# Performance work log

Measured on AMD Instinct MI355X. Metric: run time of the kernel, lower is better.

The kernel has to match this reference:

```python
import jax, jax.numpy as jnp
import numpy as np

SEED_SPACING = 0.06      # eps for DBSCAN
MIN_SAMPLES = 3          # sklearn counts the point itself
MAX_SUPERPOINTS = 512


def _dbscan_superpoints(coords):
    """DBSCAN(eps, min_samples=3) on [N,3] coords + the module's relabeling.

    Connected components over the eps-graph restricted to core points are
    found by min-index label propagation (with pointer jumping) inside a
    while_loop; border points take the min core-neighbor label; noise is
    filled with the most common label; labels are compacted and capped at
    MAX_SUPERPOINTS exactly as in the torch module. Returns [N] int32.
    """
    N = coords.shape[0]
    SENT = N  # sentinel label meaning "no cluster / noise"

    # pairwise squared euclidean distances via GEMM
    sq = jnp.sum(coords * coords, axis=-1)                      # [N]
    d2 = sq[:, None] + sq[None, :] - 2.0 * (coords @ coords.T)  # [N,N]
    adj = d2 <= SEED_SPACING * SEED_SPACING                     # includes self
    core = jnp.sum(adj, axis=-1) >= MIN_SAMPLES                 # [N] bool

    idx = jnp.arange(N)
    core_col = core[None, :]

    def step(l):
        # min label among core neighbors
        nb = jnp.min(jnp.where(adj & core_col, l[None, :], SENT), axis=-1)
        l2 = jnp.where(core, jnp.minimum(l, nb), SENT)
        # pointer jumping: labels are indices of core points, so l2[l2] is valid
        safe = jnp.where(l2 < N, l2, 0)
        l2 = jnp.where(l2 < N, jnp.minimum(l2, l2[safe]), SENT)
        return l2

    def cond(state):
        return state[1]

    def body(state):
        l, _ = state
        l_new = step(l)
        return l_new, jnp.any(l_new != l)

    l0 = jnp.where(core, idx, SENT)
    l_final, _ = jax.lax.while_loop(cond, body, (l0, jnp.array(True)))

    # border points: min label of any core neighbor; else stay noise
    border = jnp.min(jnp.where(adj & core_col, l_final[None, :], SENT), axis=-1)
    labels = jnp.where(core, l_final, border)

    # noise fill: assign most common valid label (or 0 if none valid)
    noise = labels == SENT
    safe_lab = jnp.where(noise, 0, labels)
    counts = jnp.zeros(N, jnp.int32).at[safe_lab].add(jnp.where(noise, 0, 1))
    any_valid = jnp.any(~noise)
    most_common = jnp.argmax(counts).astype(labels.dtype)
    labels = jnp.where(noise, jnp.where(any_valid, most_common, 0), labels)

    # compact to consecutive ids ordered by min point index (== first occurrence)
    present = jnp.zeros(N, bool).at[labels].set(True)
    rank = (jnp.cumsum(present) - 1).astype(labels.dtype)
    labels = rank[labels]
    n_clusters = jnp.sum(present)

    # cap at MAX_SUPERPOINTS: keep the MAX largest clusters, rest -> 0
    counts2 = jnp.zeros(N, jnp.int32).at[labels].add(1)
    top = jnp.argsort(counts2)[-MAX_SUPERPOINTS:]
    remap = jnp.zeros(N, labels.dtype).at[top].set(
        jnp.arange(MAX_SUPERPOINTS, dtype=labels.dtype))
    labels = jnp.where(n_clusters > MAX_SUPERPOINTS, remap[labels], labels)
    return labels.astype(jnp.int32)


def setup_inputs() -> dict:
    key = jax.random.key(0)
    coordinates = jax.random.uniform(key, (8, 4096, 3), dtype=jnp.float32)
    return {"coordinates": coordinates}


def reference(coordinates):
    # [B, N, 3] -> [B, N] int32 superpoint labels
    return jax.vmap(_dbscan_superpoints)(coordinates)
```

## Files before the change

kernel.cpp:

```cpp
#include <hip/hip_runtime.h>
#include <stdint.h>

#define NPTS 4096
#define SENT NPTS
#define MAXSP 512
#define ECAP 65536
#define ECACHE 16384

typedef unsigned long long ull;

__device__ __forceinline__ int find_lds(int* p, int x){
  while (true){
    int px = p[x];
    if (px == x) return x;
    int ppx = p[px];
    if (ppx == px) return px;
    p[x] = ppx;
    x = ppx;
  }
}

__device__ __forceinline__ void union_lds(int* p, int a, int b){
  a = find_lds(p, a);
  b = find_lds(p, b);
  while (a != b){
    int lo = min(a, b), hi = max(a, b);
    int old = atomicCAS(&p[hi], hi, lo);
    if (old == hi || old == lo) return;
    a = lo; b = old;
  }
}

__device__ __forceinline__ ull trimask(ull m, int i, int base){
  if (base + 63 <= i) return 0ULL;
  if (base <= i) return m & ((~0ULL) << (i - base + 1));
  return m;
}

__global__ void k_prep(const float* __restrict__ coords,
                       float4* __restrict__ pts,
                       int* __restrict__ ecnt, int batches){
#pragma clang fp contract(off)
  int g = blockIdx.x * blockDim.x + threadIdx.x;
  if (blockIdx.x == 0 && threadIdx.x < batches) ecnt[threadIdx.x << 6] = 0;
  float x = coords[g*3+0], y = coords[g*3+1], z = coords[g*3+2];
  float sq = ((x*x) + (y*y)) + (z*z);
  pts[g] = make_float4(x, y, z, sq);
}

__global__ void k_adj(const float4* __restrict__ pts,
                      uint32_t* __restrict__ edges,
                      int* __restrict__ ecnt){
#pragma clang fp contract(off)
  __shared__ int sTot, sBase;
  int tid  = threadIdx.x;
  int wv   = (blockIdx.x * blockDim.x + tid) >> 6;
  int lane = tid & 63;
  int b = wv >> 9;
  int m = wv & 511;
  int i0 = m << 2;
  int h0 = (NPTS - 4) - i0;
  const float4* pb = pts + (b << 12);
  if (tid == 0) sTot = 0;
  __syncthreads();
  const float EPS2 = (float)(0.06 * 0.06);
  float4 pL[4], pH[4];
  #pragma unroll
  for (int r = 0; r < 4; ++r){ pL[r] = pb[i0 + r]; pH[r] = pb[h0 + r]; }
  ull wl[4] = {0,0,0,0}, wh[4] = {0,0,0,0};
  int base = lane << 6;
  {
    int W = i0 >> 6;
    float4 pj = pb[(W << 6) + lane];
    for (int k = W; k < 64; ++k){
      float4 cur = pj;
      if (k + 1 < 64) pj = pb[((k + 1) << 6) + lane];
      #pragma unroll
      for (int r = 0; r < 4; ++r){
        float dot = __builtin_fmaf(pL[r].z, cur.z,
                    __builtin_fmaf(pL[r].y, cur.y, pL[r].x * cur.x));
        float d2  = __builtin_fmaf(-2.0f, dot, pL[r].w + cur.w);
        ull bal = __ballot(d2 <= EPS2);
        if (lane == k) wl[r] = bal;
      }
    }
  }
  {
    int W = h0 >> 6;
    float4 pj = pb[(W << 6) + lane];
    for (int k = W; k < 64; ++k){
      float4 cur = pj;
      if (k + 1 < 64) pj = pb[((k + 1) << 6) + lane];
      #pragma unroll
      for (int r = 0; r < 4; ++r){
        float dot = __builtin_fmaf(pH[r].z, cur.z,
                    __builtin_fmaf(pH[r].y, cur.y, pH[r].x * cur.x));
        float d2  = __builtin_fmaf(-2.0f, dot, pH[r].w + cur.w);
        ull bal = __ballot(d2 <= EPS2);
        if (lane == k) wh[r] = bal;
      }
    }
  }
  #pragma unroll
  for (int r = 0; r < 4; ++r){
    wl[r] = trimask(wl[r], i0 + r, base);
    wh[r] = trimask(wh[r], h0 + r, base);
  }
  int cnt = 0;
  #pragma unroll
  for (int r = 0; r < 4; ++r) cnt += __popcll(wl[r]) + __popcll(wh[r]);
  int incl = cnt;
  #pragma unroll
  for (int off = 1; off < 64; off <<= 1){
    int y = __shfl_up(incl, off);
    if (lane >= off) incl += y;
  }
  int total = __shfl(incl, 63);
  int woff = 0;
  if (lane == 63) woff = atomicAdd(&sTot, total);
  woff = __shfl(woff, 63);
  __syncthreads();
  if (tid == 0) sBase = atomicAdd(&ecnt[b << 6], sTot);
  __syncthreads();
  int pos = sBase + woff + incl - cnt;
  uint32_t* eb = edges + (size_t)b * ECAP;
  #define EMIT(mm, row) { ull e = (mm); while (e){ int bit = __builtin_ctzll(e); \
      e &= e - 1; if (pos < ECAP) eb[pos] = ((uint32_t)(row) << 12) | (uint32_t)(base + bit); ++pos; } }
  #pragma unroll
  for (int r = 0; r < 4; ++r) EMIT(wl[r], i0 + r)
  #pragma unroll
  for (int r = 0; r < 4; ++r) EMIT(wh[r], h0 + r)
  #undef EMIT
}

__global__ __launch_bounds__(1024) void k_mega(const uint32_t* __restrict__ edges,
                                               const int* __restrict__ ecnt,
                                               int* __restrict__ out){
  __shared__ int par[NPTS];
  __shared__ int LAB[NPTS];
  __shared__ unsigned char corea[NPTS];
  __shared__ uint32_t ec[ECACHE];
  __shared__ int wtots[16];
  __shared__ int sMost;
  int b = blockIdx.x, t = threadIdx.x;
  int wid = t >> 6, lane = t & 63;
  int cnt = min(ecnt[b << 6], ECAP);
  const uint32_t* eb = edges + (size_t)b * ECAP;
  for (int s = 0; s < 4; ++s){ int v = (t << 2) + s; par[v] = 0; }
  if (t == 0) sMost = -1;
  __syncthreads();
  for (int e = t; e < cnt; e += 1024){
    uint32_t pk = eb[e];
    if (e < ECACHE) ec[e] = pk;
    atomicAdd(&par[pk >> 12], 1);
    atomicAdd(&par[pk & 4095], 1);
  }
  __syncthreads();
  for (int s = 0; s < 4; ++s){ int v = (t << 2) + s; corea[v] = (par[v] >= 2) ? 1 : 0; }
  __syncthreads();
  for (int s = 0; s < 4; ++s){ int v = (t << 2) + s; par[v] = v; }
  __syncthreads();
  for (int e = t; e < cnt; e += 1024){
    uint32_t pk = (e < ECACHE) ? ec[e] : eb[e];
    int u = pk >> 12, v = pk & 4095;
    if (corea[u] && corea[v]) union_lds(par, u, v);
  }
  __syncthreads();
  for (int s = 0; s < 4; ++s){
    int v = (t << 2) + s;
    LAB[v] = corea[v] ? find_lds(par, v) : SENT;
  }
  __syncthreads();
  for (int e = t; e < cnt; e += 1024){
    uint32_t pk = (e < ECACHE) ? ec[e] : eb[e];
    int u = pk >> 12, v = pk & 4095;
    int cu = corea[u], cv = corea[v];
    if (cu && !cv)      atomicMin(&LAB[v], find_lds(par, u));
    else if (cv && !cu) atomicMin(&LAB[u], find_lds(par, v));
  }
  __syncthreads();
  int* A  = (int*)ec;
  int* Bb = A + NPTS;
  for (int s = 0; s < 4; ++s){ int v = (t << 2) + s; A[v] = 0; }
  __syncthreads();
  for (int s = 0; s < 4; ++s){ int l = LAB[(t << 2) + s]; if (l < SENT) atomicAdd(&A[l], 1); }
  __syncthreads();
  for (int s = 0; s < 4; ++s){
    int v = (t << 2) + s; int c = A[v];
    if (c > 0) atomicMax(&sMost, (c << 13) | (4095 - v));
  }
  __syncthreads();
  int most = (sMost >= 0) ? (4095 - (sMost & 8191)) : 0;
  for (int s = 0; s < 4; ++s){ int v = (t << 2) + s; if (LAB[v] == SENT) LAB[v] = most; Bb[v] = 0; }
  __syncthreads();
  for (int s = 0; s < 4; ++s) Bb[LAB[(t << 2) + s]] = 1;
  __syncthreads();
  int pv[4]; int ls = 0;
  for (int s = 0; s < 4; ++s){ pv[s] = Bb[(t << 2) + s]; ls += pv[s]; }
  int incl = ls;
  #pragma unroll
  for (int off = 1; off < 64; off <<= 1){
    int y = __shfl_up(incl, off);
    if (lane >= off) incl += y;
  }
  if (lane == 63) wtots[wid] = incl;
  __syncthreads();
  int wbase = 0, ncl = 0;
  #pragma unroll
  for (int w = 0; w < 16; ++w){
    int wt = wtots[w];
    if (w < wid) wbase += wt;
    ncl += wt;
  }
  int run = wbase + incl - ls;
  for (int s = 0; s < 4; ++s){ run += pv[s]; Bb[(t << 2) + s] = run - 1; }
  __syncthreads();
  for (int s = 0; s < 4; ++s){ int v = (t << 2) + s; LAB[v] = Bb[LAB[v]]; }
  __syncthreads();
  if (ncl > MAXSP){
    for (int s = 0; s < 4; ++s) A[(t << 2) + s] = 0;
    __syncthreads();
    for (int s = 0; s < 4; ++s) atomicAdd(&A[LAB[(t << 2) + s]], 1);
    __syncthreads();
    for (int v = t; v < ncl; v += 1024){
      int keyv = A[v] * NPTS + v;
      int p = 0;
      for (int u = 0; u < ncl; ++u) p += ((A[u] * NPTS + u) < keyv) ? 1 : 0;
      int full = p + (NPTS - ncl);
      Bb[v] = (full >= NPTS - MAXSP) ? (full - (NPTS - MAXSP)) : 0;
    }
    __syncthreads();
    for (int s = 0; s < 4; ++s){ int v = (t << 2) + s; LAB[v] = Bb[LAB[v]]; }
    __syncthreads();
  }
  int* og = out + (b << 12);
  for (int s = 0; s < 4; ++s){ int v = (t << 2) + s; og[v] = LAB[v]; }
}

extern "C" void kernel_launch(void* const* d_in, const int* in_sizes, int n_in,
                              void* d_out, int out_size, void* d_ws, size_t ws_size,
                              hipStream_t stream){
  const float* coords = (const float*)d_in[0];
  int* out = (int*)d_out;
  int batches = in_sizes[0] / (NPTS * 3);

  char* ws = (char*)d_ws;
  size_t off = 0;
  float4* pts = (float4*)(ws + off); off += (size_t)batches * NPTS * sizeof(float4);
  int* ecnt   = (int*)(ws + off);    off += (size_t)batches * 64 * sizeof(int);
  uint32_t* edges = (uint32_t*)(ws + off); off += (size_t)batches * ECAP * sizeof(uint32_t);

  int npts_all = batches * NPTS;
  k_prep<<<npts_all / 256, 256, 0, stream>>>(coords, pts, ecnt, batches);
  k_adj<<<npts_all / 32, 256, 0, stream>>>(pts, edges, ecnt);
  k_mega<<<batches, 1024, 0, stream>>>(edges, ecnt, out);
}
```

Before: 62.45 us.

## Fuse point prep into adjacency kernel and compute degrees with global atomics

Removes the separate prep kernel: the adjacency kernel now reads raw xyz coordinates and computes the squared norm on the fly. Per-point degree counting moves from an LDS atomic pass in the mega kernel to global atomics issued while edges are emitted, and a memset zeroes the degree and count buffers. The mega kernel drops its LDS edge cache and its first edge pass, reusing the parent array for histograms. The trade is heavier global atomic traffic, unaligned strided coordinate loads, and rereading edges from global memory in later passes.

After: 66.05 us. 1.06x slower.

```diff
diff --git a/kernel.cpp b/kernel.cpp
--- a/kernel.cpp
+++ b/kernel.cpp
@@ -5,7 +5,6 @@
 #define SENT NPTS
 #define MAXSP 512
 #define ECAP 65536
-#define ECACHE 16384
 
 typedef unsigned long long ull;
 
@@ -37,20 +36,17 @@
   return m;
 }
 
-__global__ void k_prep(const float* __restrict__ coords,
-                       float4* __restrict__ pts,
-                       int* __restrict__ ecnt, int batches){
+__device__ __forceinline__ float4 loadpt(const float* __restrict__ c, int g){
 #pragma clang fp contract(off)
-  int g = blockIdx.x * blockDim.x + threadIdx.x;
-  if (blockIdx.x == 0 && threadIdx.x < batches) ecnt[threadIdx.x << 6] = 0;
-  float x = coords[g*3+0], y = coords[g*3+1], z = coords[g*3+2];
+  float x = c[g*3+0], y = c[g*3+1], z = c[g*3+2];
   float sq = ((x*x) + (y*y)) + (z*z);
-  pts[g] = make_float4(x, y, z, sq);
-}
-
-__global__ void k_adj(const float4* __restrict__ pts,
+  return make_float4(x, y, z, sq);
+}
+
+__global__ void k_adj(const float* __restrict__ coords,
                       uint32_t* __restrict__ edges,
-                      int* __restrict__ ecnt){
+                      int* __restrict__ ecnt,
+                      int* __restrict__ deg){
 #pragma clang fp contract(off)
   __shared__ int sTot, sBase;
   int tid  = threadIdx.x;
@@ -60,21 +56,21 @@
   int m = wv & 511;
   int i0 = m << 2;
   int h0 = (NPTS - 4) - i0;
-  const float4* pb = pts + (b << 12);
+  const float* cb = coords + ((size_t)b << 12) * 3;
   if (tid == 0) sTot = 0;
   __syncthreads();
   const float EPS2 = (float)(0.06 * 0.06);
   float4 pL[4], pH[4];
   #pragma unroll
-  for (int r = 0; r < 4; ++r){ pL[r] = pb[i0 + r]; pH[r] = pb[h0 + r]; }
+  for (int r = 0; r < 4; ++r){ pL[r] = loadpt(cb, i0 + r); pH[r] = loadpt(cb, h0 + r); }
   ull wl[4] = {0,0,0,0}, wh[4] = {0,0,0,0};
   int base = lane << 6;
   {
     int W = i0 >> 6;
-    float4 pj = pb[(W << 6) + lane];
+    float4 pj = loadpt(cb, (W << 6) + lane);
     for (int k = W; k < 64; ++k){
       float4 cur = pj;
-      if (k + 1 < 64) pj = pb[((k + 1) << 6) + lane];
+      if (k + 1 < 64) pj = loadpt(cb, ((k + 1) << 6) + lane);
       #pragma unroll
       for (int r = 0; r < 4; ++r){
         float dot = __builtin_fmaf(pL[r].z, cur.z,
@@ -87,10 +83,10 @@
   }
   {
     int W = h0 >> 6;
-    float4 pj = pb[(W << 6) + lane];
+    float4 pj = loadpt(cb, (W << 6) + lane);
     for (int k = W; k < 64; ++k){
       float4 cur = pj;
-      if (k + 1 < 64) pj = pb[((k + 1) << 6) + lane];
+      if (k + 1 < 64) pj = loadpt(cb, ((k + 1) << 6) + lane);
       #pragma unroll
       for (int r = 0; r < 4; ++r){
         float dot = __builtin_fmaf(pH[r].z, cur.z,
@@ -124,8 +120,11 @@
   __syncthreads();
   int pos = sBase + woff + incl - cnt;
   uint32_t* eb = edges + (size_t)b * ECAP;
+  int* dg = deg + (b << 12);
   #define EMIT(mm, row) { ull e = (mm); while (e){ int bit = __builtin_ctzll(e); \
-      e &= e - 1; if (pos < ECAP) eb[pos] = ((uint32_t)(row) << 12) | (uint32_t)(base + bit); ++pos; } }
+      e &= e - 1; int j = base + bit; \
+      if (pos < ECAP) eb[pos] = ((uint32_t)(row) << 12) | (uint32_t)j; ++pos; \
+      atomicAdd(&dg[row], 1); atomicAdd(&dg[j], 1); } }
   #pragma unroll
   for (int r = 0; r < 4; ++r) EMIT(wl[r], i0 + r)
   #pragma unroll
@@ -135,33 +134,28 @@
 
 __global__ __launch_bounds__(1024) void k_mega(const uint32_t* __restrict__ edges,
                                                const int* __restrict__ ecnt,
+                                               const int* __restrict__ deg,
                                                int* __restrict__ out){
   __shared__ int par[NPTS];
   __shared__ int LAB[NPTS];
+  __shared__ int Bb[NPTS];
   __shared__ unsigned char corea[NPTS];
-  __shared__ uint32_t ec[ECACHE];
   __shared__ int wtots[16];
   __shared__ int sMost;
   int b = blockIdx.x, t = threadIdx.x;
   int wid = t >> 6, lane = t & 63;
   int cnt = min(ecnt[b << 6], ECAP);
   const uint32_t* eb = edges + (size_t)b * ECAP;
-  for (int s = 0; s < 4; ++s){ int v = (t << 2) + s; par[v] = 0; }
+  const int* dg = deg + (b << 12);
+  for (int s = 0; s < 4; ++s){
+    int v = (t << 2) + s;
+    corea[v] = (dg[v] >= 2) ? 1 : 0;
+    par[v] = v;
+  }
   if (t == 0) sMost = -1;
   __syncthreads();
   for (int e = t; e < cnt; e += 1024){
     uint32_t pk = eb[e];
-    if (e < ECACHE) ec[e] = pk;
-    atomicAdd(&par[pk >> 12], 1);
-    atomicAdd(&par[pk & 4095], 1);
-  }
-  __syncthreads();
-  for (int s = 0; s < 4; ++s){ int v = (t << 2) + s; corea[v] = (par[v] >= 2) ? 1 : 0; }
-  __syncthreads();
-  for (int s = 0; s < 4; ++s){ int v = (t << 2) + s; par[v] = v; }
-  __syncthreads();
-  for (int e = t; e < cnt; e += 1024){
-    uint32_t pk = (e < ECACHE) ? ec[e] : eb[e];
     int u = pk >> 12, v = pk & 4095;
     if (corea[u] && corea[v]) union_lds(par, u, v);
   }
@@ -172,15 +166,14 @@
   }
   __syncthreads();
   for (int e = t; e < cnt; e += 1024){
-    uint32_t pk = (e < ECACHE) ? ec[e] : eb[e];
+    uint32_t pk = eb[e];
     int u = pk >> 12, v = pk & 4095;
     int cu = corea[u], cv = corea[v];
     if (cu && !cv)      atomicMin(&LAB[v], find_lds(par, u));
     else if (cv && !cu) atomicMin(&LAB[u], find_lds(par, v));
   }
   __syncthreads();
-  int* A  = (int*)ec;
-  int* Bb = A + NPTS;
+  int* A = par;
   for (int s = 0; s < 4; ++s){ int v = (t << 2) + s; A[v] = 0; }
   __syncthreads();
   for (int s = 0; s < 4; ++s){ int l = LAB[(t << 2) + s]; if (l < SENT) atomicAdd(&A[l], 1); }
@@ -246,12 +239,13 @@
 
   char* ws = (char*)d_ws;
   size_t off = 0;
-  float4* pts = (float4*)(ws + off); off += (size_t)batches * NPTS * sizeof(float4);
-  int* ecnt   = (int*)(ws + off);    off += (size_t)batches * 64 * sizeof(int);
+  int* deg  = (int*)(ws + off); off += (size_t)batches * NPTS * sizeof(int);
+  int* ecnt = (int*)(ws + off); off += (size_t)batches * 64 * sizeof(int);
+  size_t zbytes = off;
   uint32_t* edges = (uint32_t*)(ws + off); off += (size_t)batches * ECAP * sizeof(uint32_t);
 
   int npts_all = batches * NPTS;
-  k_prep<<<npts_all / 256, 256, 0, stream>>>(coords, pts, ecnt, batches);
-  k_adj<<<npts_all / 32, 256, 0, stream>>>(pts, edges, ecnt);
-  k_mega<<<batches, 1024, 0, stream>>>(edges, ecnt, out);
-}
+  hipMemsetAsync(ws, 0, zbytes, stream);
+  k_adj<<<npts_all / 32, 256, 0, stream>>>(coords, edges, ecnt, deg);
+  k_mega<<<batches, 1024, 0, stream>>>(edges, ecnt, deg, out);
+}
```
